# Optimization experiments

Measured on AMD Instinct MI355X. Metric: run time of the kernel, lower is better.

The kernel has to match this reference:

```python
import jax, jax.numpy as jnp
import numpy as np

B, A, D, H = 256, 16, 768, 512
LN_EPS = 1e-5


def setup_inputs() -> dict:
    key = jax.random.key(0)
    ks = jax.random.split(key, 8)
    aspects = jax.random.normal(ks[0], (B, A, D), dtype=jnp.float32)
    aspect_mask = jnp.ones((B, A), dtype=bool)
    # relation_gate: Linear(2D->H), ReLU, Dropout(eval=id), Linear(H->1)
    # xavier_uniform with gain=0.1, bias=-2.0 (per the module's custom init)
    lim1 = 0.1 * np.sqrt(6.0 / (2 * D + H))
    lim2 = 0.1 * np.sqrt(6.0 / (H + 1))
    W_g1 = jax.random.uniform(ks[1], (2 * D, H), jnp.float32, -lim1, lim1)
    b_g1 = jnp.full((H,), -2.0, dtype=jnp.float32)
    w_g2 = jax.random.uniform(ks[2], (H,), jnp.float32, -lim2, lim2)
    b_g2 = jnp.asarray(-2.0, dtype=jnp.float32)
    # composition: Linear(2D->H), ReLU, Dropout(eval=id), Linear(H->D), default init scale
    sc1 = 1.0 / np.sqrt(2 * D)
    sc2 = 1.0 / np.sqrt(H)
    W_c1 = jax.random.uniform(ks[3], (2 * D, H), jnp.float32, -sc1, sc1)
    b_c1 = jax.random.uniform(ks[4], (H,), jnp.float32, -sc1, sc1)
    W_c2 = jax.random.uniform(ks[5], (H, D), jnp.float32, -sc2, sc2)
    b_c2 = jax.random.uniform(ks[6], (D,), jnp.float32, -sc2, sc2)
    ln_gamma = jnp.ones((D,), dtype=jnp.float32)
    ln_beta = jnp.zeros((D,), dtype=jnp.float32)
    return {
        "aspects": aspects, "aspect_mask": aspect_mask,
        "W_g1": W_g1, "b_g1": b_g1, "w_g2": w_g2, "b_g2": b_g2,
        "W_c1": W_c1, "b_c1": b_c1, "W_c2": W_c2, "b_c2": b_c2,
        "ln_gamma": ln_gamma, "ln_beta": ln_beta,
    }


def reference(aspects, aspect_mask, W_g1, b_g1, w_g2, b_g2,
              W_c1, b_c1, W_c2, b_c2, ln_gamma, ln_beta):
    b, a, d = aspects.shape
    # cat([x_i, x_j]) @ W == x_i @ W[:D] + x_j @ W[D:]  -> batch all (i,j) pairs at once
    Wg_i, Wg_j = W_g1[:d], W_g1[d:]
    gi = jnp.einsum('bad,dh->bah', aspects, Wg_i)   # [B,A,H]
    gj = jnp.einsum('bad,dh->bah', aspects, Wg_j)   # [B,A,H]
    hg = jax.nn.relu(gi[:, :, None, :] + gj[:, None, :, :] + b_g1)  # [B,A,A,H]
    gate = jax.nn.sigmoid(jnp.einsum('bijh,h->bij', hg, w_g2) + b_g2)  # [B,A,A]
    eye = jnp.eye(a, dtype=bool)
    gate = jnp.where(eye[None], 0.0, gate)  # i==j pair skipped; all_gates diag stays 0

    Wc_i, Wc_j = W_c1[:d], W_c1[d:]
    ci = jnp.einsum('bad,dh->bah', aspects, Wc_i)
    cj = jnp.einsum('bad,dh->bah', aspects, Wc_j)
    hc = jax.nn.relu(ci[:, :, None, :] + cj[:, None, :, :] + b_c1)  # [B,A,A,H]
    composed = jnp.einsum('bijh,hd->bijd', hc, W_c2) + b_c2          # [B,A,A,D]
    # gated sum over source aspects j (gate is 0 on diag, masking i==j)
    influence = jnp.einsum('bij,bijd->bid', gate, composed)
    final = aspects + influence
    # LayerNorm over last dim
    mu = jnp.mean(final, axis=-1, keepdims=True)
    var = jnp.mean(jnp.square(final - mu), axis=-1, keepdims=True)
    final = (final - mu) * jax.lax.rsqrt(var + LN_EPS) * ln_gamma + ln_beta
    final = final * aspect_mask[..., None].astype(final.dtype)
    return final, gate
```

## Files before the change

kernel.cpp:

```cpp
#include <hip/hip_runtime.h>
#include <stdint.h>
#include <stddef.h>

typedef __attribute__((ext_vector_type(8))) short bf16x8;
typedef __attribute__((ext_vector_type(4))) float f32x4;
typedef __attribute__((ext_vector_type(8))) unsigned short u16x8;

typedef __attribute__((address_space(1))) unsigned int as1_u32;
typedef __attribute__((address_space(3))) unsigned int as3_u32;

__device__ __forceinline__ unsigned short f2b(float f) {
  union { unsigned int u; float f; } v; v.f = f;
  unsigned int u = v.u;
  return (unsigned short)((u + 0x7FFFu + ((u >> 16) & 1u)) >> 16);
}
__device__ __forceinline__ float b2f(unsigned short s) {
  union { unsigned int u; float f; } v; v.u = ((unsigned int)s) << 16; return v.f;
}
__device__ __forceinline__ void gld16(const unsigned short* g, unsigned short* l) {
  __builtin_amdgcn_global_load_lds((const as1_u32*)(unsigned int*)(size_t)(const void*)g,
                                   (as3_u32*)(unsigned int*)l, 16, 0, 0);
}

#define LN_EPS 1e-5f
#define BB 256
#define AA 16
#define DD 768
#define HH 512
#define ASTR 776

__global__ __launch_bounds__(256) void prep(const float* __restrict__ Wg1,
                                            const float* __restrict__ Wc1,
                                            const float* __restrict__ Wc2,
                                            const float* __restrict__ aspects,
                                            unsigned short* __restrict__ Wt,
                                            unsigned short* __restrict__ Wc2t,
                                            unsigned short* __restrict__ Abf) {
  const int seg = blockIdx.z;
  if (seg == 5) {
    const int id = (blockIdx.y * 24 + blockIdx.x) * 256 + threadIdx.x + threadIdx.y * 32;
    for (int g = id; g < 393216; g += 147456) {
      const size_t i = (size_t)g * 8;
      const float4 f0 = *(const float4*)(aspects + i);
      const float4 f1 = *(const float4*)(aspects + i + 4);
      u16x8 p;
      p[0] = f2b(f0.x); p[1] = f2b(f0.y); p[2] = f2b(f0.z); p[3] = f2b(f0.w);
      p[4] = f2b(f1.x); p[5] = f2b(f1.y); p[6] = f2b(f1.z); p[7] = f2b(f1.w);
      *(u16x8*)(Abf + i) = p;
    }
    return;
  }
  const float* src;
  unsigned short* dst;
  int R, C;
  if (seg < 4) {
    src = (seg < 2 ? Wg1 : Wc1) + (size_t)(seg & 1) * DD * HH;
    dst = Wt + (size_t)seg * HH * DD;
    R = DD; C = HH;
  } else {
    src = Wc2; dst = Wc2t; R = HH; C = DD;
  }
  const int c0 = blockIdx.x * 32, r0 = blockIdx.y * 32;
  if (c0 >= C || r0 >= R) return;
  __shared__ float t[32][33];
  const int x = threadIdx.x;
  for (int yy = threadIdx.y; yy < 32; yy += 8)
    t[yy][x] = src[(size_t)(r0 + yy) * C + (c0 + x)];
  __syncthreads();
  for (int yy = threadIdx.y; yy < 32; yy += 8)
    dst[(size_t)(c0 + yy) * R + (r0 + x)] = f2b(t[x][yy]);
}

__global__ __launch_bounds__(256) void gemm1(const unsigned short* __restrict__ A,
                                             const unsigned short* __restrict__ Bt,
                                             unsigned short* __restrict__ P) {
  const int bx = blockIdx.x;
  const int mb = bx & 31, nb = bx >> 5;
  const int tid = threadIdx.x;
  const int w = tid >> 6, lane = tid & 63;
  const int lr = lane & 15, quad = lane >> 4;
  const int m0 = (w & 1) * 64, n0 = (w >> 1) * 64;
  const int K = DD;

  __shared__ __align__(16) unsigned short As[128 * 64];
  __shared__ __align__(16) unsigned short Bs[128 * 64];

  f32x4 acc[4][4] = {};

  const unsigned short* gsrc[8];
  unsigned short* lbase[8];
#pragma unroll
  for (int i = 0; i < 8; ++i) {
    const int cb = w * 64 + i * 256;
    const int c = cb + lane;
    if (cb < 1024) {
      const int row = c >> 3, lcol = (c & 7) ^ (row & 7);
      gsrc[i]  = A + (size_t)(mb * 128 + row) * K + lcol * 8;
      lbase[i] = As + cb * 8;
    } else {
      const int p = c - 1024, row = p >> 3, lcol = (p & 7) ^ (row & 7);
      gsrc[i]  = Bt + (size_t)(nb * 128 + row) * K + lcol * 8;
      lbase[i] = Bs + (cb - 1024) * 8;
    }
  }

  for (int kk = 0; kk < K; kk += 64) {
    __syncthreads();
#pragma unroll
    for (int i = 0; i < 8; ++i) gld16(gsrc[i] + kk, lbase[i]);
    __syncthreads();
#pragma unroll
    for (int h = 0; h < 2; ++h) {
      bf16x8 a4[4], b4[4];
#pragma unroll
      for (int i = 0; i < 4; ++i) {
        const int row = m0 + i * 16 + lr;
        a4[i] = *(const bf16x8*)(As + row * 64 + (((quad + h * 4) ^ (row & 7)) * 8));
      }
#pragma unroll
      for (int j = 0; j < 4; ++j) {
        const int row = n0 + j * 16 + lr;
        b4[j] = *(const bf16x8*)(Bs + row * 64 + (((quad + h * 4) ^ (row & 7)) * 8));
      }
#pragma unroll
      for (int i = 0; i < 4; ++i)
#pragma unroll
        for (int j = 0; j < 4; ++j)
          acc[i][j] = __builtin_amdgcn_mfma_f32_16x16x32_bf16(a4[i], b4[j], acc[i][j], 0, 0, 0);
    }
  }

  const int rowb = mb * 128 + m0 + quad * 4;
  const int colb = nb * 128 + n0 + lr;
#pragma unroll
  for (int i = 0; i < 4; ++i)
#pragma unroll
    for (int j = 0; j < 4; ++j)
#pragma unroll
      for (int r = 0; r < 4; ++r)
        P[(size_t)(rowb + i * 16 + r) * 2048 + colb + j * 16] = f2b(acc[i][j][r]);
}

__global__ __launch_bounds__(512) void pairwise(const unsigned short* __restrict__ P,
                                                const float* __restrict__ bg1,
                                                const float* __restrict__ wg2,
                                                const float* __restrict__ bg2p,
                                                const float* __restrict__ bc1,
                                                unsigned short* __restrict__ u,
                                                float* __restrict__ gsum,
                                                float* __restrict__ gateO) {
  const int b = blockIdx.x;
  const int tid = threadIdx.x;
  const int v = tid >> 6;
  const int lane = tid & 63;
  __shared__ unsigned short S[16 * 2048];
  const unsigned short* Pb = P + (size_t)b * 16 * 2048;
#pragma unroll
  for (int i = 0; i < 8; ++i) {
    const int off = (tid + i * 512) * 8;
    *(u16x8*)(S + off) = *(const u16x8*)(Pb + off);
  }
  __syncthreads();

  float bg1v[8], wg2v[8], bc1v[8];
#pragma unroll
  for (int q = 0; q < 8; ++q) {
    const int h = lane + q * 64;
    bg1v[q] = bg1[h]; wg2v[q] = wg2[h]; bc1v[q] = bc1[h];
  }
  const float bg2s = bg2p[0];

  float giR[2][8], ciR[2][8];
#pragma unroll
  for (int r = 0; r < 2; ++r) {
    const int i = v * 2 + r;
#pragma unroll
    for (int q = 0; q < 8; ++q) {
      const int h = lane + q * 64;
      giR[r][q] = b2f(S[i * 2048 + h]);
      ciR[r][q] = b2f(S[i * 2048 + 1024 + h]);
    }
  }

  float uac[2][8] = {};
  float gs[2] = {0.f, 0.f};
  for (int j = 0; j < AA; ++j) {
    float gjq[8], cjq[8];
#pragma unroll
    for (int q = 0; q < 8; ++q) {
      const int h = lane + q * 64;
      gjq[q] = b2f(S[j * 2048 + 512 + h]);
      cjq[q] = b2f(S[j * 2048 + 1536 + h]);
    }
#pragma unroll
    for (int r = 0; r < 2; ++r) {
      const int i = v * 2 + r;
      float dot = 0.f;
#pragma unroll
      for (int q = 0; q < 8; ++q)
        dot = fmaf(fmaxf(giR[r][q] + gjq[q] + bg1v[q], 0.f), wg2v[q], dot);
#pragma unroll
      for (int off = 32; off; off >>= 1) dot += __shfl_xor(dot, off);
      float gate = (j == i) ? 0.f : (1.f / (1.f + __expf(-(dot + bg2s))));
      if (lane == 0) gateO[((size_t)b * 16 + i) * 16 + j] = gate;
      gs[r] += gate;
#pragma unroll
      for (int q = 0; q < 8; ++q)
        uac[r][q] = fmaf(gate, fmaxf(ciR[r][q] + cjq[q] + bc1v[q], 0.f), uac[r][q]);
    }
  }
#pragma unroll
  for (int r = 0; r < 2; ++r) {
    const int i = v * 2 + r;
#pragma unroll
    for (int q = 0; q < 8; ++q)
      u[(size_t)(b * 16 + i) * HH + lane + q * 64] = f2b(uac[r][q]);
    if (lane == 0) gsum[b * 16 + i] = gs[r];
  }
}

__global__ __launch_bounds__(512) void gemm2ln(const unsigned short* __restrict__ u,
                                               const unsigned short* __restrict__ Wc2t,
                                               const float* __restrict__ gsum,
                                               const float* __restrict__ aspects,
                                               const float* __restrict__ bc2,
                                               const float* __restrict__ gma,
                                               const float* __restrict__ bta,
                                               float* __restrict__ outF) {
  const int b = blockIdx.x;
  const int tid = threadIdx.x;
  const int v = tid >> 6;
  const int lane = tid & 63;
  const int lr = lane & 15, quad = lane >> 4;

  __shared__ float buf[4704];
  unsigned short* uS = (unsigned short*)buf;
  float* redS = buf + 4160;
  float* musS = buf + 4416;
  float* rsS  = buf + 4432;

  const unsigned short* ub = u + (size_t)b * 16 * HH;
#pragma unroll
  for (int it = 0; it < 2; ++it) {
    const int t = tid + it * 512;
    const int row = t >> 6, off = (t & 63) * 8;
    *(u16x8*)(uS + row * 520 + off) = *(const u16x8*)(ub + row * HH + off);
  }
  __syncthreads();

  f32x4 oc[6] = {};
  {
    const unsigned short* up = uS + lr * 520 + quad * 8;
    const unsigned short* wp = Wc2t + (size_t)(v * 96 + lr) * HH + quad * 8;
    bf16x8 c6[6], n6[6];
#pragma unroll
    for (int t = 0; t < 6; ++t) c6[t] = *(const bf16x8*)(wp + (size_t)t * (16 * HH));
    for (int kk = 0; kk < HH; kk += 64) {
#pragma unroll
      for (int t = 0; t < 6; ++t) n6[t] = *(const bf16x8*)(wp + (size_t)t * (16 * HH) + kk + 32);
      {
        bf16x8 af = *(const bf16x8*)(up + kk);
#pragma unroll
        for (int t = 0; t < 6; ++t)
          oc[t] = __builtin_amdgcn_mfma_f32_16x16x32_bf16(af, c6[t], oc[t], 0, 0, 0);
      }
      if (kk + 64 < HH) {
#pragma unroll
        for (int t = 0; t < 6; ++t) c6[t] = *(const bf16x8*)(wp + (size_t)t * (16 * HH) + kk + 64);
      }
      {
        bf16x8 af = *(const bf16x8*)(up + kk + 32);
#pragma unroll
        for (int t = 0; t < 6; ++t)
          oc[t] = __builtin_amdgcn_mfma_f32_16x16x32_bf16(af, n6[t], oc[t], 0, 0, 0);
      }
    }
  }

  float val[6][4];
  float s1p[4] = {0.f, 0.f, 0.f, 0.f}, s2p[4] = {0.f, 0.f, 0.f, 0.f};
  const int R0 = quad * 4;
  float gsv[4];
#pragma unroll
  for (int r = 0; r < 4; ++r) gsv[r] = gsum[(size_t)b * 16 + R0 + r];
#pragma unroll
  for (int t = 0; t < 6; ++t) {
    const int n = v * 96 + t * 16 + lr;
    const float bc2v = bc2[n];
#pragma unroll
    for (int r = 0; r < 4; ++r) {
      const size_t m = (size_t)b * 16 + R0 + r;
      const float x = oc[t][r] + gsv[r] * bc2v + aspects[m * DD + n];
      val[t][r] = x;
      s1p[r] += x;
      s2p[r] = fmaf(x, x, s2p[r]);
    }
  }
#pragma unroll
  for (int off = 8; off; off >>= 1)
#pragma unroll
    for (int r = 0; r < 4; ++r) {
      s1p[r] += __shfl_xor(s1p[r], off);
      s2p[r] += __shfl_xor(s2p[r], off);
    }
  if (lr == 0) {
#pragma unroll
    for (int r = 0; r < 4; ++r) {
      redS[(v * 16 + R0 + r) * 2 + 0] = s1p[r];
      redS[(v * 16 + R0 + r) * 2 + 1] = s2p[r];
    }
  }
  __syncthreads();
  if (tid < 16) {
    float s1 = 0.f, s2 = 0.f;
#pragma unroll
    for (int w = 0; w < 8; ++w) {
      s1 += redS[(w * 16 + tid) * 2 + 0];
      s2 += redS[(w * 16 + tid) * 2 + 1];
    }
    const float mu = s1 * (1.f / 768.f);
    const float var = s2 * (1.f / 768.f) - mu * mu;
    musS[tid] = mu;
    rsS[tid] = rsqrtf(var + LN_EPS);
  }
  __syncthreads();
#pragma unroll
  for (int t = 0; t < 6; ++t) {
    const int n = v * 96 + t * 16 + lr;
    const float g = gma[n], be = bta[n];
#pragma unroll
    for (int r = 0; r < 4; ++r) {
      const int row = R0 + r;
      outF[((size_t)b * 16 + row) * DD + n] = (val[t][r] - musS[row]) * rsS[row] * g + be;
    }
  }
}

extern "C" void kernel_launch(void* const* d_in, const int* in_sizes, int n_in,
                              void* d_out, int out_size, void* d_ws, size_t ws_size,
                              hipStream_t stream) {
  const float* aspects = (const float*)d_in[0];
  const float* W_g1 = (const float*)d_in[2];
  const float* b_g1 = (const float*)d_in[3];
  const float* w_g2 = (const float*)d_in[4];
  const float* b_g2 = (const float*)d_in[5];
  const float* W_c1 = (const float*)d_in[6];
  const float* b_c1 = (const float*)d_in[7];
  const float* W_c2 = (const float*)d_in[8];
  const float* b_c2 = (const float*)d_in[9];
  const float* ln_g = (const float*)d_in[10];
  const float* ln_b = (const float*)d_in[11];

  float* outF  = (float*)d_out;
  float* gateO = outF + (size_t)BB * AA * DD;

  char* ws = (char*)d_ws;
  unsigned short* Wt   = (unsigned short*)ws;
  unsigned short* Wc2t = (unsigned short*)(ws + 3145728);
  unsigned short* Abf  = (unsigned short*)(ws + 3932160);
  unsigned short* P    = (unsigned short*)(ws + 10223616);
  unsigned short* u    = (unsigned short*)(ws + 27000832);
  float* gsum          = (float*)(ws + 31195136);

  prep<<<dim3(24, 24, 6), dim3(32, 8, 1), 0, stream>>>(W_g1, W_c1, W_c2, aspects,
                                                       Wt, Wc2t, Abf);
  gemm1<<<512, 256, 0, stream>>>(Abf, Wt, P);
  pairwise<<<BB, 512, 0, stream>>>(P, b_g1, w_g2, b_g2, b_c1, u, gsum, gateO);
  gemm2ln<<<BB, 512, 0, stream>>>(u, Wc2t, gsum, aspects, b_c2, ln_g, ln_b, outF);
}
```

Baseline: 153.9 us.

## Fuse pairwise and GEMM2+LayerNorm kernels; double-buffer gemm1 LDS loads

Merges the pairwise gate/accumulate kernel with the second GEMM and LayerNorm kernel, so the u and gsum intermediates stay in shared memory and one launch plus a global round trip go away. The gemm1 K-loop gets double-buffered LDS with prefetch of the next tile and explicit waitcnt and barrier calls, to overlap global loads with MFMA work. The pairwise loads also change: P goes straight into LDS with global_load_lds, the bias vectors are read as float4, and the LDS reads are vectorised, which changes which h index each lane owns. In exchange gemm1 uses twice the LDS (64KB), which may lower occupancy.

```diff
diff --git a/kernel.cpp b/kernel.cpp
--- a/kernel.cpp
+++ b/kernel.cpp
@@ -27,7 +27,6 @@
 #define AA 16
 #define DD 768
 #define HH 512
-#define ASTR 776
 
 __global__ __launch_bounds__(256) void prep(const float* __restrict__ Wg1,
                                             const float* __restrict__ Wc1,
@@ -82,33 +81,43 @@
   const int m0 = (w & 1) * 64, n0 = (w >> 1) * 64;
   const int K = DD;
 
-  __shared__ __align__(16) unsigned short As[128 * 64];
-  __shared__ __align__(16) unsigned short Bs[128 * 64];
+  __shared__ __align__(16) unsigned short Ls[2][16384];
 
   f32x4 acc[4][4] = {};
 
   const unsigned short* gsrc[8];
-  unsigned short* lbase[8];
+  int loff[8];
 #pragma unroll
   for (int i = 0; i < 8; ++i) {
     const int cb = w * 64 + i * 256;
     const int c = cb + lane;
     if (cb < 1024) {
       const int row = c >> 3, lcol = (c & 7) ^ (row & 7);
-      gsrc[i]  = A + (size_t)(mb * 128 + row) * K + lcol * 8;
-      lbase[i] = As + cb * 8;
+      gsrc[i] = A + (size_t)(mb * 128 + row) * K + lcol * 8;
+      loff[i] = cb * 8;
     } else {
       const int p = c - 1024, row = p >> 3, lcol = (p & 7) ^ (row & 7);
-      gsrc[i]  = Bt + (size_t)(nb * 128 + row) * K + lcol * 8;
-      lbase[i] = Bs + (cb - 1024) * 8;
-    }
-  }
-
+      gsrc[i] = Bt + (size_t)(nb * 128 + row) * K + lcol * 8;
+      loff[i] = (cb - 1024) * 8 + 8192;
+    }
+  }
+
+#pragma unroll
+  for (int i = 0; i < 8; ++i) gld16(gsrc[i], Ls[0] + loff[i]);
+
+  int cur = 0;
   for (int kk = 0; kk < K; kk += 64) {
-    __syncthreads();
-#pragma unroll
-    for (int i = 0; i < 8; ++i) gld16(gsrc[i] + kk, lbase[i]);
-    __syncthreads();
+    if (kk + 64 < K) {
+#pragma unroll
+      for (int i = 0; i < 8; ++i) gld16(gsrc[i] + kk + 64, Ls[cur ^ 1] + loff[i]);
+      asm volatile("s_waitcnt vmcnt(8)" ::: "memory");
+    } else {
+      asm volatile("s_waitcnt vmcnt(0)" ::: "memory");
+    }
+    __builtin_amdgcn_s_barrier();
+
+    const unsigned short* As = Ls[cur];
+    const unsigned short* Bs = Ls[cur] + 8192;
 #pragma unroll
     for (int h = 0; h < 2; ++h) {
       bf16x8 a4[4], b4[4];
@@ -128,6 +137,9 @@
         for (int j = 0; j < 4; ++j)
           acc[i][j] = __builtin_amdgcn_mfma_f32_16x16x32_bf16(a4[i], b4[j], acc[i][j], 0, 0, 0);
     }
+    asm volatile("s_waitcnt lgkmcnt(0)" ::: "memory");
+    __builtin_amdgcn_s_barrier();
+    cur ^= 1;
   }
 
   const int rowb = mb * 128 + m0 + quad * 4;
@@ -141,110 +153,96 @@
         P[(size_t)(rowb + i * 16 + r) * 2048 + colb + j * 16] = f2b(acc[i][j][r]);
 }
 
-__global__ __launch_bounds__(512) void pairwise(const unsigned short* __restrict__ P,
-                                                const float* __restrict__ bg1,
-                                                const float* __restrict__ wg2,
-                                                const float* __restrict__ bg2p,
-                                                const float* __restrict__ bc1,
-                                                unsigned short* __restrict__ u,
-                                                float* __restrict__ gsum,
-                                                float* __restrict__ gateO) {
-  const int b = blockIdx.x;
-  const int tid = threadIdx.x;
-  const int v = tid >> 6;
-  const int lane = tid & 63;
-  __shared__ unsigned short S[16 * 2048];
-  const unsigned short* Pb = P + (size_t)b * 16 * 2048;
-#pragma unroll
-  for (int i = 0; i < 8; ++i) {
-    const int off = (tid + i * 512) * 8;
-    *(u16x8*)(S + off) = *(const u16x8*)(Pb + off);
-  }
-  __syncthreads();
-
-  float bg1v[8], wg2v[8], bc1v[8];
-#pragma unroll
-  for (int q = 0; q < 8; ++q) {
-    const int h = lane + q * 64;
-    bg1v[q] = bg1[h]; wg2v[q] = wg2[h]; bc1v[q] = bc1[h];
-  }
-  const float bg2s = bg2p[0];
-
-  float giR[2][8], ciR[2][8];
-#pragma unroll
-  for (int r = 0; r < 2; ++r) {
-    const int i = v * 2 + r;
-#pragma unroll
-    for (int q = 0; q < 8; ++q) {
-      const int h = lane + q * 64;
-      giR[r][q] = b2f(S[i * 2048 + h]);
-      ciR[r][q] = b2f(S[i * 2048 + 1024 + h]);
-    }
-  }
-
-  float uac[2][8] = {};
-  float gs[2] = {0.f, 0.f};
-  for (int j = 0; j < AA; ++j) {
-    float gjq[8], cjq[8];
-#pragma unroll
-    for (int q = 0; q < 8; ++q) {
-      const int h = lane + q * 64;
-      gjq[q] = b2f(S[j * 2048 + 512 + h]);
-      cjq[q] = b2f(S[j * 2048 + 1536 + h]);
-    }
-#pragma unroll
-    for (int r = 0; r < 2; ++r) {
-      const int i = v * 2 + r;
-      float dot = 0.f;
-#pragma unroll
-      for (int q = 0; q < 8; ++q)
-        dot = fmaf(fmaxf(giR[r][q] + gjq[q] + bg1v[q], 0.f), wg2v[q], dot);
-#pragma unroll
-      for (int off = 32; off; off >>= 1) dot += __shfl_xor(dot, off);
-      float gate = (j == i) ? 0.f : (1.f / (1.f + __expf(-(dot + bg2s))));
-      if (lane == 0) gateO[((size_t)b * 16 + i) * 16 + j] = gate;
-      gs[r] += gate;
-#pragma unroll
-      for (int q = 0; q < 8; ++q)
-        uac[r][q] = fmaf(gate, fmaxf(ciR[r][q] + cjq[q] + bc1v[q], 0.f), uac[r][q]);
-    }
-  }
-#pragma unroll
-  for (int r = 0; r < 2; ++r) {
-    const int i = v * 2 + r;
-#pragma unroll
-    for (int q = 0; q < 8; ++q)
-      u[(size_t)(b * 16 + i) * HH + lane + q * 64] = f2b(uac[r][q]);
-    if (lane == 0) gsum[b * 16 + i] = gs[r];
-  }
-}
-
-__global__ __launch_bounds__(512) void gemm2ln(const unsigned short* __restrict__ u,
-                                               const unsigned short* __restrict__ Wc2t,
-                                               const float* __restrict__ gsum,
-                                               const float* __restrict__ aspects,
-                                               const float* __restrict__ bc2,
-                                               const float* __restrict__ gma,
-                                               const float* __restrict__ bta,
-                                               float* __restrict__ outF) {
+__global__ __launch_bounds__(512) void pairfused(
+    const unsigned short* __restrict__ P,
+    const float* __restrict__ bg1, const float* __restrict__ wg2,
+    const float* __restrict__ bg2p, const float* __restrict__ bc1,
+    const unsigned short* __restrict__ Wc2t,
+    const float* __restrict__ aspects, const float* __restrict__ bc2,
+    const float* __restrict__ gma, const float* __restrict__ bta,
+    float* __restrict__ outF, float* __restrict__ gateO) {
   const int b = blockIdx.x;
   const int tid = threadIdx.x;
   const int v = tid >> 6;
   const int lane = tid & 63;
   const int lr = lane & 15, quad = lane >> 4;
 
-  __shared__ float buf[4704];
-  unsigned short* uS = (unsigned short*)buf;
-  float* redS = buf + 4160;
-  float* musS = buf + 4416;
-  float* rsS  = buf + 4432;
-
-  const unsigned short* ub = u + (size_t)b * 16 * HH;
-#pragma unroll
-  for (int it = 0; it < 2; ++it) {
-    const int t = tid + it * 512;
-    const int row = t >> 6, off = (t & 63) * 8;
-    *(u16x8*)(uS + row * 520 + off) = *(const u16x8*)(ub + row * HH + off);
+  __shared__ __align__(16) unsigned short S[16 * 2048];
+  unsigned short* uS = S;
+  float* fb   = (float*)((char*)S + 16640);
+  float* redS = fb;
+  float* musS = fb + 256;
+  float* rsS  = fb + 272;
+  float* gsS  = fb + 288;
+
+  const unsigned short* Pb = P + (size_t)b * 16 * 2048;
+#pragma unroll
+  for (int i = 0; i < 8; ++i) {
+    const int off = (tid + i * 512) * 8;
+    gld16(Pb + off, S + off);
+  }
+
+  float bg1v[8], wg2v[8], bc1v[8];
+  {
+    const int h0 = lane * 8;
+    const float4 a0 = *(const float4*)(bg1 + h0), a1 = *(const float4*)(bg1 + h0 + 4);
+    const float4 b0 = *(const float4*)(wg2 + h0), b1 = *(const float4*)(wg2 + h0 + 4);
+    const float4 c0 = *(const float4*)(bc1 + h0), c1 = *(const float4*)(bc1 + h0 + 4);
+    bg1v[0] = a0.x; bg1v[1] = a0.y; bg1v[2] = a0.z; bg1v[3] = a0.w;
+    bg1v[4] = a1.x; bg1v[5] = a1.y; bg1v[6] = a1.z; bg1v[7] = a1.w;
+    wg2v[0] = b0.x; wg2v[1] = b0.y; wg2v[2] = b0.z; wg2v[3] = b0.w;
+    wg2v[4] = b1.x; wg2v[5] = b1.y; wg2v[6] = b1.z; wg2v[7] = b1.w;
+    bc1v[0] = c0.x; bc1v[1] = c0.y; bc1v[2] = c0.z; bc1v[3] = c0.w;
+    bc1v[4] = c1.x; bc1v[5] = c1.y; bc1v[6] = c1.z; bc1v[7] = c1.w;
+  }
+  const float bg2s = bg2p[0];
+  __syncthreads();
+
+  float giR[2][8], ciR[2][8];
+#pragma unroll
+  for (int r = 0; r < 2; ++r) {
+    const int i = v * 2 + r;
+    const u16x8 g8 = *(const u16x8*)(S + i * 2048 + lane * 8);
+    const u16x8 c8 = *(const u16x8*)(S + i * 2048 + 1024 + lane * 8);
+#pragma unroll
+    for (int q = 0; q < 8; ++q) { giR[r][q] = b2f(g8[q]); ciR[r][q] = b2f(c8[q]); }
+  }
+
+  float uac[2][8] = {};
+  float gs[2] = {0.f, 0.f};
+  for (int j = 0; j < AA; ++j) {
+    const u16x8 gj8 = *(const u16x8*)(S + j * 2048 + 512 + lane * 8);
+    const u16x8 cj8 = *(const u16x8*)(S + j * 2048 + 1536 + lane * 8);
+    float gjq[8], cjq[8];
+#pragma unroll
+    for (int q = 0; q < 8; ++q) { gjq[q] = b2f(gj8[q]); cjq[q] = b2f(cj8[q]); }
+#pragma unroll
+    for (int r = 0; r < 2; ++r) {
+      const int i = v * 2 + r;
+      float dot = 0.f;
+#pragma unroll
+      for (int q = 0; q < 8; ++q)
+        dot = fmaf(fmaxf(giR[r][q] + gjq[q] + bg1v[q], 0.f), wg2v[q], dot);
+#pragma unroll
+      for (int off = 32; off; off >>= 1) dot += __shfl_xor(dot, off);
+      const float gate = (j == i) ? 0.f : (1.f / (1.f + __expf(-(dot + bg2s))));
+      if (lane == 0) gateO[((size_t)b * 16 + i) * 16 + j] = gate;
+      gs[r] += gate;
+#pragma unroll
+      for (int q = 0; q < 8; ++q)
+        uac[r][q] = fmaf(gate, fmaxf(ciR[r][q] + cjq[q] + bc1v[q], 0.f), uac[r][q]);
+    }
+  }
+  __syncthreads();
+
+#pragma unroll
+  for (int r = 0; r < 2; ++r) {
+    const int i = v * 2 + r;
+    u16x8 pk;
+#pragma unroll
+    for (int q = 0; q < 8; ++q) pk[q] = f2b(uac[r][q]);
+    *(u16x8*)(uS + i * 520 + lane * 8) = pk;
+    if (lane == 0) gsS[i] = gs[r];
   }
   __syncthreads();
 
@@ -259,7 +257,7 @@
 #pragma unroll
       for (int t = 0; t < 6; ++t) n6[t] = *(const bf16x8*)(wp + (size_t)t * (16 * HH) + kk + 32);
       {
-        bf16x8 af = *(const bf16x8*)(up + kk);
+        const bf16x8 af = *(const bf16x8*)(up + kk);
 #pragma unroll
         for (int t = 0; t < 6; ++t)
           oc[t] = __builtin_amdgcn_mfma_f32_16x16x32_bf16(af, c6[t], oc[t], 0, 0, 0);
@@ -269,7 +267,7 @@
         for (int t = 0; t < 6; ++t) c6[t] = *(const bf16x8*)(wp + (size_t)t * (16 * HH) + kk + 64);
       }
       {
-        bf16x8 af = *(const bf16x8*)(up + kk + 32);
+        const bf16x8 af = *(const bf16x8*)(up + kk + 32);
 #pragma unroll
         for (int t = 0; t < 6; ++t)
           oc[t] = __builtin_amdgcn_mfma_f32_16x16x32_bf16(af, n6[t], oc[t], 0, 0, 0);
@@ -282,7 +280,7 @@
   const int R0 = quad * 4;
   float gsv[4];
 #pragma unroll
-  for (int r = 0; r < 4; ++r) gsv[r] = gsum[(size_t)b * 16 + R0 + r];
+  for (int r = 0; r < 4; ++r) gsv[r] = gsS[R0 + r];
 #pragma unroll
   for (int t = 0; t < 6; ++t) {
     const int n = v * 96 + t * 16 + lr;
@@ -359,12 +357,10 @@
   unsigned short* Wc2t = (unsigned short*)(ws + 3145728);
   unsigned short* Abf  = (unsigned short*)(ws + 3932160);
   unsigned short* P    = (unsigned short*)(ws + 10223616);
-  unsigned short* u    = (unsigned short*)(ws + 27000832);
-  float* gsum          = (float*)(ws + 31195136);
 
   prep<<<dim3(24, 24, 6), dim3(32, 8, 1), 0, stream>>>(W_g1, W_c1, W_c2, aspects,
                                                        Wt, Wc2t, Abf);
   gemm1<<<512, 256, 0, stream>>>(Abf, Wt, P);
-  pairwise<<<BB, 512, 0, stream>>>(P, b_g1, w_g2, b_g2, b_c1, u, gsum, gateO);
-  gemm2ln<<<BB, 512, 0, stream>>>(u, Wc2t, gsum, aspects, b_c2, ln_g, ln_b, outF);
-}
+  pairfused<<<BB, 512, 0, stream>>>(P, b_g1, w_g2, b_g2, b_c1, Wc2t, aspects,
+                                    b_c2, ln_g, ln_b, outF, gateO);
+}
```

Result: faster. 146.1 us (-5.0%).
